# Performance work log

Hardware: AMD Instinct MI355X
Metric: run time of the kernel (lower is better)

## Reference

```python
import jax, jax.numpy as jnp
import numpy as np

B, S, D, H = 2, 2048, 1024, 16  # batch, seq_len, model dim, heads


def setup_inputs() -> dict:
    key = jax.random.key(0)
    ks = jax.random.split(key, 5)
    return {
        "x": jax.random.normal(ks[0], (B, S, D), jnp.float32),
        "idx": jax.random.randint(ks[1], (B,), 0, S),
        "weight": jnp.float32(0.5),
        "attn_forcing": 1,  # static python flag
        "w_qkv": jax.random.normal(ks[2], (D, 3 * D), jnp.float32) * 0.02,
        "b_qkv": jnp.zeros((3 * D,), jnp.float32),
        "w_proj": jax.random.normal(ks[3], (D, D), jnp.float32) * 0.02,
        "b_proj": jnp.zeros((D,), jnp.float32),
    }


def reference(x, idx, weight, attn_forcing, w_qkv, b_qkv, w_proj, b_proj):
    Bx, Sx, Dm = x.shape
    dh = Dm // H
    # qkv projection (Conv1D: x @ w + b)
    qkv = x @ w_qkv + b_qkv  # [B,S,3D]
    q, k, v = jnp.split(qkv, 3, axis=-1)
    q = q.reshape(Bx, Sx, H, dh).transpose(0, 2, 1, 3)  # [B,H,S,dh]
    k = k.reshape(Bx, Sx, H, dh).transpose(0, 2, 1, 3)
    v = v.reshape(Bx, Sx, H, dh).transpose(0, 2, 1, 3)
    alen = jnp.arange(Sx)
    mask = (alen[None, :] <= alen[:, None]).astype(x.dtype)  # [S,S] causal
    w = jnp.einsum('bhqd,bhkd->bhqk', q, k) / jnp.asarray(np.sqrt(dh), x.dtype)
    w = w * mask + jnp.asarray(-1e9, x.dtype) * (1 - mask)
    w = jax.nn.softmax(w, axis=-1)
    if attn_forcing:
        # post-softmax forcing reweight: positions >= idx scaled by weight, then renorm
        a = jnp.where(alen[None, :] >= idx[:, None], weight, jnp.asarray(1.0, x.dtype))  # [B,S]
        w = w * a[:, None, None, :]
        w = w / jnp.sum(w, axis=-1, keepdims=True)
    out = jnp.einsum('bhqk,bhkd->bhqd', w, v)  # [B,H,S,dh]
    out = out.transpose(0, 2, 1, 3).reshape(Bx, Sx, Dm)  # merge heads
    return out @ w_proj + b_proj
```

## Files before the change

kernel.cpp:

```cpp
#include <hip/hip_runtime.h>


typedef __attribute__((ext_vector_type(8))) short short8;
typedef __attribute__((ext_vector_type(4))) float f32x4;

#define MFMA_B16(a, b, c) __builtin_amdgcn_mfma_f32_16x16x32_bf16(a, b, c, 0, 0, 0)

static __device__ __forceinline__ unsigned short f2bf(float f) {
    union { float f; unsigned int u; } v;
    v.f = f;
    unsigned int r = (v.u + 0x7fffu + ((v.u >> 16) & 1u)) >> 16;
    return (unsigned short)r;
}

static __device__ __forceinline__ unsigned int pk_bf16(float a, float b) {
#if __has_builtin(__builtin_amdgcn_cvt_pk_bf16_f32)
    typedef __bf16 bf2 __attribute__((ext_vector_type(2)));
    union { bf2 v; unsigned int u; } c;
    c.v = __builtin_amdgcn_cvt_pk_bf16_f32(a, b);
    return c.u;
#else
    return (unsigned int)f2bf(a) | ((unsigned int)f2bf(b) << 16);
#endif
}

static __device__ __forceinline__ void gl_lds16(const void* g, void* l) {
    __builtin_amdgcn_global_load_lds(
        (const __attribute__((address_space(1))) unsigned int*)g,
        (__attribute__((address_space(3))) unsigned int*)l, 16, 0, 0);
}

__global__ __launch_bounds__(256) void convert_x_kernel(const float4* __restrict__ x,
                                                        ushort4* __restrict__ xb) {
    int i = blockIdx.x * 256 + threadIdx.x;
    float4 v = x[i];
    ushort4 o;
    o.x = f2bf(v.x); o.y = f2bf(v.y); o.z = f2bf(v.z); o.w = f2bf(v.w);
    xb[i] = o;
}

__global__ __launch_bounds__(256) void transpose_cvt_kernel(const float* __restrict__ in,
                                                            unsigned short* __restrict__ out,
                                                            int R, int C) {
    __shared__ float t[32][33];
    int c0 = blockIdx.x * 32, r0 = blockIdx.y * 32;
    int x = threadIdx.x, y = threadIdx.y;
    #pragma unroll
    for (int yy = y; yy < 32; yy += 8)
        t[yy][x] = in[(size_t)(r0 + yy) * C + (c0 + x)];
    __syncthreads();
    #pragma unroll
    for (int yy = y; yy < 32; yy += 8)
        out[(size_t)(c0 + yy) * R + (r0 + x)] = f2bf(t[x][yy]);
}

__global__ __launch_bounds__(256) void transpose_v_kernel(const unsigned short* __restrict__ v,
                                                          unsigned short* __restrict__ vT) {
    __shared__ unsigned short t[32][33];
    int d0 = blockIdx.x * 32, s0 = blockIdx.y * 32, bh = blockIdx.z;
    const unsigned short* vb = v + (size_t)bh * 2048 * 64;
    unsigned short* vTb = vT + (size_t)bh * 2048 * 64;
    int x = threadIdx.x, y = threadIdx.y;
    #pragma unroll
    for (int yy = y; yy < 32; yy += 8)
        t[yy][x] = vb[(s0 + yy) * 64 + d0 + x];
    __syncthreads();
    #pragma unroll
    for (int yy = y; yy < 32; yy += 8)
        vTb[(d0 + yy) * 2048 + s0 + x] = t[x][yy];
}

__global__ __launch_bounds__(256) void gemm_qkv_kernel(const unsigned short* __restrict__ A,
                                                       const unsigned short* __restrict__ Bt,
                                                       const float* __restrict__ bias,
                                                       unsigned short* __restrict__ q,
                                                       unsigned short* __restrict__ k,
                                                       unsigned short* __restrict__ v) {
    __shared__ unsigned short As[128 * 64];
    __shared__ unsigned short Bs[128 * 64];
    const int tid = threadIdx.x;
    const int lane = tid & 63, wave = tid >> 6;
    const int l15 = lane & 15, quad = lane >> 4;
    const int wm = wave >> 1, wn = wave & 1;
    const int row0 = blockIdx.y * 128, col0 = blockIdx.x * 128;
    const int K = 1024;

    int srow[4], scol[4], sdst[4];
    #pragma unroll
    for (int h = 0; h < 4; ++h) {
        int D = h * 256 + wave * 64 + lane;
        srow[h] = D >> 3;
        scol[h] = ((D & 7) ^ (srow[h] & 7)) * 8;
        sdst[h] = (h * 256 + wave * 64) * 8;
    }

    f32x4 acc[4][4] = {};

    for (int kt = 0; kt < K; kt += 64) {
        #pragma unroll
        for (int h = 0; h < 4; ++h) {
            gl_lds16(&A[(size_t)(row0 + srow[h]) * K + kt + scol[h]], &As[sdst[h]]);
            gl_lds16(&Bt[(size_t)(col0 + srow[h]) * K + kt + scol[h]], &Bs[sdst[h]]);
        }
        __syncthreads();
        #pragma unroll
        for (int kk = 0; kk < 2; ++kk) {
            short8 af[4], bf[4];
            #pragma unroll
            for (int i = 0; i < 4; ++i) {
                int r = wm * 64 + i * 16 + l15;
                af[i] = *(const short8*)&As[r * 64 + (((kk * 4 + quad) ^ (r & 7)) * 8)];
            }
            #pragma unroll
            for (int j = 0; j < 4; ++j) {
                int r = wn * 64 + j * 16 + l15;
                bf[j] = *(const short8*)&Bs[r * 64 + (((kk * 4 + quad) ^ (r & 7)) * 8)];
            }
            #pragma unroll
            for (int i = 0; i < 4; ++i)
                #pragma unroll
                for (int j = 0; j < 4; ++j)
                    acc[i][j] = MFMA_B16(af[i], bf[j], acc[i][j]);
        }
        __syncthreads();
    }

    #pragma unroll
    for (int i = 0; i < 4; ++i)
        #pragma unroll
        for (int j = 0; j < 4; ++j)
            #pragma unroll
            for (int r = 0; r < 4; ++r) {
                int row = row0 + wm * 64 + i * 16 + quad * 4 + r;
                int col = col0 + wn * 64 + j * 16 + l15;
                float val = acc[i][j][r] + bias[col];
                int which = col >> 10, rem = col & 1023;
                int hh = rem >> 6, d = rem & 63;
                int b = row >> 11, s = row & 2047;
                size_t o = ((size_t)((b * 16 + hh) * 2048 + s)) * 64 + d;
                if (which == 0) q[o] = f2bf(val * 0.125f);
                else if (which == 1) k[o] = f2bf(val);
                else v[o] = f2bf(val);
            }
}

__global__ __launch_bounds__(256) void gemm_proj_kernel(const unsigned short* __restrict__ A,
                                                        const unsigned short* __restrict__ Bt,
                                                        const float* __restrict__ bias,
                                                        float* __restrict__ out) {
    __shared__ unsigned short As[128 * 64];
    __shared__ unsigned short Bs[64 * 64];
    const int tid = threadIdx.x;
    const int lane = tid & 63, wave = tid >> 6;
    const int l15 = lane & 15, quad = lane >> 4;
    const int wm = wave >> 1, wn = wave & 1;
    const int row0 = blockIdx.y * 128, col0 = blockIdx.x * 64;
    const int K = 1024;

    int srow[4], scol[4], sdst[4];
    #pragma unroll
    for (int h = 0; h < 4; ++h) {
        int D = h * 256 + wave * 64 + lane;
        srow[h] = D >> 3;
        scol[h] = ((D & 7) ^ (srow[h] & 7)) * 8;
        sdst[h] = (h * 256 + wave * 64) * 8;
    }

    f32x4 acc[4][2] = {};

    for (int kt = 0; kt < K; kt += 64) {
        #pragma unroll
        for (int h = 0; h < 4; ++h)
            gl_lds16(&A[(size_t)(row0 + srow[h]) * K + kt + scol[h]], &As[sdst[h]]);
        #pragma unroll
        for (int h = 0; h < 2; ++h)
            gl_lds16(&Bt[(size_t)(col0 + srow[h]) * K + kt + scol[h]], &Bs[sdst[h]]);
        __syncthreads();
        #pragma unroll
        for (int kk = 0; kk < 2; ++kk) {
            short8 af[4], bf[2];
            #pragma unroll
            for (int i = 0; i < 4; ++i) {
                int r = wm * 64 + i * 16 + l15;
                af[i] = *(const short8*)&As[r * 64 + (((kk * 4 + quad) ^ (r & 7)) * 8)];
            }
            #pragma unroll
            for (int j = 0; j < 2; ++j) {
                int r = wn * 32 + j * 16 + l15;
                bf[j] = *(const short8*)&Bs[r * 64 + (((kk * 4 + quad) ^ (r & 7)) * 8)];
            }
            #pragma unroll
            for (int i = 0; i < 4; ++i)
                #pragma unroll
                for (int j = 0; j < 2; ++j)
                    acc[i][j] = MFMA_B16(af[i], bf[j], acc[i][j]);
        }
        __syncthreads();
    }

    #pragma unroll
    for (int i = 0; i < 4; ++i)
        #pragma unroll
        for (int j = 0; j < 2; ++j)
            #pragma unroll
            for (int r = 0; r < 4; ++r) {
                int row = row0 + wm * 64 + i * 16 + quad * 4 + r;
                int col = col0 + wn * 32 + j * 16 + l15;
                out[(size_t)row * 1024 + col] = acc[i][j][r] + bias[col];
            }
}

__global__ __launch_bounds__(256) void attn_kernel(const unsigned short* __restrict__ Q,
                                                   const unsigned short* __restrict__ Kg,
                                                   const unsigned short* __restrict__ Vt,
                                                   const int* __restrict__ idx,
                                                   const float* __restrict__ weight,
                                                   const int* __restrict__ forcing,
                                                   unsigned short* __restrict__ O) {
    __shared__ unsigned short Ks[2][4096];
    __shared__ unsigned short Vs[2][4096];
    __shared__ unsigned short Pw[4][1024];

    const int tid = threadIdx.x;
    const int lane = tid & 63, wave = tid >> 6;
    const int l15 = lane & 15, quad = lane >> 4;
    const int bid = blockIdx.x;
    const int u = bid >> 5, a = u & 7, qg = u >> 3;
    const int t = (qg == 0) ? (31 - a) : (qg == 1) ? (16 + a) : (qg == 2) ? (15 - a) : a;
    const int bh = bid & 31;
    const int b = bh >> 4, hh = bh & 15;
    const unsigned short* Qb = Q + (size_t)bh * 2048 * 64;
    const unsigned short* Kh = Kg + (size_t)bh * 2048 * 64;
    const unsigned short* Vh = Vt + (size_t)bh * 2048 * 64;

    const int idxb = idx[b];
    const float wgt = (forcing[0] != 0) ? weight[0] : 1.0f;

    const int L0 = wave * 128 + lane;
    const int rS = L0 >> 3;
    const int cS = (L0 & 7) ^ (rS & 7);
    const int ldsOffJ0 = (wave * 128) * 8;
    const int ldsOffJ1 = (wave * 128 + 64) * 8;

    const int q0 = t * 64 + wave * 16;
    const int qrow = q0 + l15;

    short8 aq0 = *(const short8*)&Qb[(q0 + l15) * 64 + quad * 8];
    short8 aq1 = *(const short8*)&Qb[(q0 + l15) * 64 + 32 + quad * 8];

    float m = -3.0e38f, l = 0.0f;
    f32x4 o[4] = {};

    const int nkb = t + 1;

    {
        const unsigned short* kg = Kh + (size_t)rS * 64 + cS * 8;
        const unsigned short* vg = Vh + (size_t)rS * 2048 + cS * 8;
        gl_lds16(kg,            &Ks[0][ldsOffJ0]);
        gl_lds16(kg + 8 * 64,   &Ks[0][ldsOffJ1]);
        gl_lds16(vg,            &Vs[0][ldsOffJ0]);
        gl_lds16(vg + 8 * 2048, &Vs[0][ldsOffJ1]);
    }
    __syncthreads();

    unsigned short* const pwb = &Pw[wave][0];
    const int pwr = l15 * 64;
    const int pa7 = l15 & 7;

    for (int kb = 0; kb < nkb; ++kb) {
        const int cur = kb & 1;
        const int kbase = kb * 64;
        if (kb + 1 < nkb) {
            const int nb = kbase + 64;
            const unsigned short* kg = Kh + (size_t)(nb + rS) * 64 + cS * 8;
            const unsigned short* vg = Vh + (size_t)rS * 2048 + nb + cS * 8;
            gl_lds16(kg,            &Ks[cur ^ 1][ldsOffJ0]);
            gl_lds16(kg + 8 * 64,   &Ks[cur ^ 1][ldsOffJ1]);
            gl_lds16(vg,            &Vs[cur ^ 1][ldsOffJ0]);
            gl_lds16(vg + 8 * 2048, &Vs[cur ^ 1][ldsOffJ1]);
        }

        f32x4 sT[4];
        #pragma unroll
        for (int kt = 0; kt < 4; ++kt) {
            const int row = kt * 16 + l15;
            short8 k0 = *(const short8*)&Ks[cur][row * 64 + ((quad ^ (row & 7)) * 8)];
            short8 k1 = *(const short8*)&Ks[cur][row * 64 + (((4 + quad) ^ (row & 7)) * 8)];
            f32x4 z = {};
            z = MFMA_B16(k0, aq0, z);
            z = MFMA_B16(k1, aq1, z);
            sT[kt] = z;
        }

        if (kb == t) {
            #pragma unroll
            for (int kt = 0; kt < 4; ++kt)
                #pragma unroll
                for (int r = 0; r < 4; ++r)
                    if (kbase + kt * 16 + quad * 4 + r > qrow) sT[kt][r] = -3.0e38f;
        }

        float mloc = fmaxf(fmaxf(fmaxf(sT[0][0], sT[0][1]), fmaxf(sT[0][2], sT[0][3])),
                           fmaxf(fmaxf(sT[1][0], sT[1][1]), fmaxf(sT[1][2], sT[1][3])));
        mloc = fmaxf(mloc, fmaxf(fmaxf(fmaxf(sT[2][0], sT[2][1]), fmaxf(sT[2][2], sT[2][3])),
                                 fmaxf(fmaxf(sT[3][0], sT[3][1]), fmaxf(sT[3][2], sT[3][3]))));
        mloc = fmaxf(mloc, __shfl_xor(mloc, 16));
        mloc = fmaxf(mloc, __shfl_xor(mloc, 32));
        const float mnew = fmaxf(m, mloc);
        const float alpha = __expf(m - mnew);
        m = mnew;

        #pragma unroll
        for (int kt = 0; kt < 4; ++kt)
            #pragma unroll
            for (int r = 0; r < 4; ++r)
                sT[kt][r] = __expf(sT[kt][r] - mnew);
        if (kbase >= idxb) {
            #pragma unroll
            for (int kt = 0; kt < 4; ++kt)
                #pragma unroll
                for (int r = 0; r < 4; ++r) sT[kt][r] *= wgt;
        } else if (kbase + 63 >= idxb) {
            #pragma unroll
            for (int kt = 0; kt < 4; ++kt)
                #pragma unroll
                for (int r = 0; r < 4; ++r)
                    if (kbase + kt * 16 + quad * 4 + r >= idxb) sT[kt][r] *= wgt;
        }

        float rs = ((sT[0][0] + sT[0][1]) + (sT[0][2] + sT[0][3])) +
                   ((sT[1][0] + sT[1][1]) + (sT[1][2] + sT[1][3])) +
                   ((sT[2][0] + sT[2][1]) + (sT[2][2] + sT[2][3])) +
                   ((sT[3][0] + sT[3][1]) + (sT[3][2] + sT[3][3]));
        rs += __shfl_xor(rs, 16);
        rs += __shfl_xor(rs, 32);
        l = l * alpha + rs;

        #pragma unroll
        for (int dt = 0; dt < 4; ++dt) {
            f32x4 tt = o[dt];
            #pragma unroll
            for (int r = 0; r < 4; ++r) tt[r] *= alpha;
            o[dt] = tt;
        }

        #pragma unroll
        for (int kt = 0; kt < 4; ++kt) {
            unsigned int* pw = (unsigned int*)&pwb[pwr +
                (((kt * 2 + (quad >> 1)) ^ pa7) * 8) + (quad & 1) * 4];
            pw[0] = pk_bf16(sT[kt][0], sT[kt][1]);
            pw[1] = pk_bf16(sT[kt][2], sT[kt][3]);
        }

        short8 bp0 = *(const short8*)&pwb[pwr + ((quad ^ pa7) * 8)];
        short8 bp1 = *(const short8*)&pwb[pwr + (((4 + quad) ^ pa7) * 8)];

        #pragma unroll
        for (int dt = 0; dt < 4; ++dt) {
            const int row = dt * 16 + l15;
            short8 vf0 = *(const short8*)&Vs[cur][row * 64 + ((quad ^ (row & 7)) * 8)];
            short8 vf1 = *(const short8*)&Vs[cur][row * 64 + (((4 + quad) ^ (row & 7)) * 8)];
            f32x4 oo = o[dt];
            oo = MFMA_B16(vf0, bp0, oo);
            oo = MFMA_B16(vf1, bp1, oo);
            o[dt] = oo;
        }

        __syncthreads();
    }

    const float inv = 1.0f / l;
    unsigned short* sc = &Ks[0][0] + wave * 1152;
    #pragma unroll
    for (int dt = 0; dt < 4; ++dt)
        #pragma unroll
        for (int r = 0; r < 4; ++r)
            sc[l15 * 72 + dt * 16 + quad * 4 + r] = f2bf(o[dt][r] * inv);
    const size_t rowoff = ((size_t)(b * 2048 + q0 + l15)) * 1024 + hh * 64;
    #pragma unroll
    for (int h = 0; h < 2; ++h) {
        short8 v8 = *(const short8*)&sc[l15 * 72 + quad * 16 + h * 8];
        *(short8*)&O[rowoff + quad * 16 + h * 8] = v8;
    }
}

extern "C" void kernel_launch(void* const* d_in, const int* in_sizes, int n_in,
                              void* d_out, int out_size, void* d_ws, size_t ws_size,
                              hipStream_t stream) {
    const float* x        = (const float*)d_in[0];
    const int*   idx      = (const int*)d_in[1];
    const float* weight   = (const float*)d_in[2];
    const int*   forcing  = (const int*)d_in[3];
    const float* w_qkv    = (const float*)d_in[4];
    const float* b_qkv    = (const float*)d_in[5];
    const float* w_proj   = (const float*)d_in[6];
    const float* b_proj   = (const float*)d_in[7];
    float* out = (float*)d_out;

    char* ws = (char*)d_ws;
    unsigned short* xb      = (unsigned short*)(ws);
    unsigned short* wqkvT   = (unsigned short*)(ws + 8388608);
    unsigned short* wprojT  = (unsigned short*)(ws + 14680064);
    unsigned short* qbuf    = (unsigned short*)(ws + 16777216);
    unsigned short* kbuf    = (unsigned short*)(ws + 25165824);
    unsigned short* vbuf    = (unsigned short*)(ws + 33554432);
    unsigned short* vTbuf   = (unsigned short*)(ws + 41943040);
    unsigned short* attn_out = xb;

    convert_x_kernel<<<4096, 256, 0, stream>>>((const float4*)x, (ushort4*)xb);
    transpose_cvt_kernel<<<dim3(96, 32), dim3(32, 8), 0, stream>>>(w_qkv, wqkvT, 1024, 3072);
    transpose_cvt_kernel<<<dim3(32, 32), dim3(32, 8), 0, stream>>>(w_proj, wprojT, 1024, 1024);
    gemm_qkv_kernel<<<dim3(24, 32), 256, 0, stream>>>(xb, wqkvT, b_qkv, qbuf, kbuf, vbuf);
    transpose_v_kernel<<<dim3(2, 64, 32), dim3(32, 8), 0, stream>>>(vbuf, vTbuf);
    attn_kernel<<<1024, 256, 0, stream>>>(qbuf, kbuf, vTbuf, idx, weight, forcing, attn_out);
    gemm_proj_kernel<<<dim3(16, 32), 256, 0, stream>>>(attn_out, wprojT, b_proj, out);
}
```

Measured before the change: 210.1 us.

## Fuse V transpose into QKV GEMM epilogue and drop online-softmax max tracking

```diff
diff --git a/kernel.cpp b/kernel.cpp
--- a/kernel.cpp
+++ b/kernel.cpp
@@ -5,6 +5,12 @@
 typedef __attribute__((ext_vector_type(4))) float f32x4;
 
 #define MFMA_B16(a, b, c) __builtin_amdgcn_mfma_f32_16x16x32_bf16(a, b, c, 0, 0, 0)
+
+#if __has_builtin(__builtin_amdgcn_exp2f)
+#define EXP2(x) __builtin_amdgcn_exp2f(x)
+#else
+#define EXP2(x) exp2f(x)
+#endif
 
 static __device__ __forceinline__ unsigned short f2bf(float f) {
     union { float f; unsigned int u; } v;
@@ -54,28 +60,12 @@
         out[(size_t)(c0 + yy) * R + (r0 + x)] = f2bf(t[x][yy]);
 }
 
-__global__ __launch_bounds__(256) void transpose_v_kernel(const unsigned short* __restrict__ v,
-                                                          unsigned short* __restrict__ vT) {
-    __shared__ unsigned short t[32][33];
-    int d0 = blockIdx.x * 32, s0 = blockIdx.y * 32, bh = blockIdx.z;
-    const unsigned short* vb = v + (size_t)bh * 2048 * 64;
-    unsigned short* vTb = vT + (size_t)bh * 2048 * 64;
-    int x = threadIdx.x, y = threadIdx.y;
-    #pragma unroll
-    for (int yy = y; yy < 32; yy += 8)
-        t[yy][x] = vb[(s0 + yy) * 64 + d0 + x];
-    __syncthreads();
-    #pragma unroll
-    for (int yy = y; yy < 32; yy += 8)
-        vTb[(d0 + yy) * 2048 + s0 + x] = t[x][yy];
-}
-
 __global__ __launch_bounds__(256) void gemm_qkv_kernel(const unsigned short* __restrict__ A,
                                                        const unsigned short* __restrict__ Bt,
                                                        const float* __restrict__ bias,
                                                        unsigned short* __restrict__ q,
                                                        unsigned short* __restrict__ k,
-                                                       unsigned short* __restrict__ v) {
+                                                       unsigned short* __restrict__ vT) {
     __shared__ unsigned short As[128 * 64];
     __shared__ unsigned short Bs[128 * 64];
     const int tid = threadIdx.x;
@@ -125,23 +115,54 @@
         __syncthreads();
     }
 
-    #pragma unroll
-    for (int i = 0; i < 4; ++i)
-        #pragma unroll
-        for (int j = 0; j < 4; ++j)
-            #pragma unroll
-            for (int r = 0; r < 4; ++r) {
-                int row = row0 + wm * 64 + i * 16 + quad * 4 + r;
-                int col = col0 + wn * 64 + j * 16 + l15;
-                float val = acc[i][j][r] + bias[col];
-                int which = col >> 10, rem = col & 1023;
-                int hh = rem >> 6, d = rem & 63;
-                int b = row >> 11, s = row & 2047;
-                size_t o = ((size_t)((b * 16 + hh) * 2048 + s)) * 64 + d;
-                if (which == 0) q[o] = f2bf(val * 0.125f);
-                else if (which == 1) k[o] = f2bf(val);
-                else v[o] = f2bf(val);
-            }
+    const int b = row0 >> 11;
+    const int srow0 = row0 & 2047;
+
+    if (blockIdx.x < 16) {
+        #pragma unroll
+        for (int i = 0; i < 4; ++i)
+            #pragma unroll
+            for (int j = 0; j < 4; ++j)
+                #pragma unroll
+                for (int r = 0; r < 4; ++r) {
+                    int row = row0 + wm * 64 + i * 16 + quad * 4 + r;
+                    int col = col0 + wn * 64 + j * 16 + l15;
+                    float val = acc[i][j][r] + bias[col];
+                    int which = col >> 10, rem = col & 1023;
+                    int hh = rem >> 6, d = rem & 63;
+                    int s = row & 2047;
+                    size_t o = ((size_t)((b * 16 + hh) * 2048 + s)) * 64 + d;
+                    if (which == 0) q[o] = f2bf(val * 0.1803368867f);
+                    else k[o] = f2bf(val);
+                }
+    } else {
+        unsigned short* tb = (wn == 0) ? As : Bs;
+        #pragma unroll
+        for (int i = 0; i < 4; ++i)
+            #pragma unroll
+            for (int j = 0; j < 4; ++j) {
+                const int col6 = j * 16 + l15;
+                const int gcol = col0 + wn * 64 + col6;
+                const float bb = bias[gcol];
+                const int chunk = wm * 8 + i * 2 + (quad >> 1);
+                unsigned int* pw = (unsigned int*)&tb[col6 * 128 +
+                    ((chunk ^ (col6 & 15)) * 8) + (quad & 1) * 4];
+                pw[0] = pk_bf16(acc[i][j][0] + bb, acc[i][j][1] + bb);
+                pw[1] = pk_bf16(acc[i][j][2] + bb, acc[i][j][3] + bb);
+            }
+        __syncthreads();
+        const int c = tid >> 1;
+        const int half = c >> 6, col6 = c & 63;
+        const int rhalf = (tid & 1) * 64;
+        const unsigned short* src = half ? Bs : As;
+        const int hh = (blockIdx.x - 16) * 2 + half;
+        unsigned short* dst = vT + ((size_t)((b * 16 + hh) * 64 + col6)) * 2048 + srow0 + rhalf;
+        #pragma unroll
+        for (int kk = 0; kk < 8; ++kk) {
+            const int chunk = ((rhalf >> 3) + kk) ^ (col6 & 15);
+            *(short8*)&dst[kk * 8] = *(const short8*)&src[col6 * 128 + chunk * 8];
+        }
+    }
 }
 
 __global__ __launch_bounds__(256) void gemm_proj_kernel(const unsigned short* __restrict__ A,
@@ -234,7 +255,7 @@
     const unsigned short* Vh = Vt + (size_t)bh * 2048 * 64;
 
     const int idxb = idx[b];
-    const float wgt = (forcing[0] != 0) ? weight[0] : 1.0f;
+    const float lw = (forcing[0] != 0) ? __log2f(weight[0]) : 0.0f;
 
     const int L0 = wave * 128 + lane;
     const int rS = L0 >> 3;
@@ -248,8 +269,10 @@
     short8 aq0 = *(const short8*)&Qb[(q0 + l15) * 64 + quad * 8];
     short8 aq1 = *(const short8*)&Qb[(q0 + l15) * 64 + 32 + quad * 8];
 
-    float m = -3.0e38f, l = 0.0f;
+    const short8 ones8 = {0x3F80, 0x3F80, 0x3F80, 0x3F80, 0x3F80, 0x3F80, 0x3F80, 0x3F80};
+
     f32x4 o[4] = {};
+    f32x4 lsum = {};
 
     const int nkb = t + 1;
 
@@ -280,13 +303,24 @@
             gl_lds16(vg + 8 * 2048, &Vs[cur ^ 1][ldsOffJ1]);
         }
 
+        const bool fullF = (kbase >= idxb);
+        const bool bndF = (!fullF) && (kbase + 63 >= idxb);
+        const float zu = fullF ? lw : 0.0f;
+
         f32x4 sT[4];
         #pragma unroll
         for (int kt = 0; kt < 4; ++kt) {
             const int row = kt * 16 + l15;
             short8 k0 = *(const short8*)&Ks[cur][row * 64 + ((quad ^ (row & 7)) * 8)];
             short8 k1 = *(const short8*)&Ks[cur][row * 64 + (((4 + quad) ^ (row & 7)) * 8)];
-            f32x4 z = {};
+            f32x4 z;
+            if (!bndF) {
+                z[0] = zu; z[1] = zu; z[2] = zu; z[3] = zu;
+            } else {
+                #pragma unroll
+                for (int r = 0; r < 4; ++r)
+                    z[r] = (kbase + kt * 16 + quad * 4 + r >= idxb) ? lw : 0.0f;
+            }
             z = MFMA_B16(k0, aq0, z);
             z = MFMA_B16(k1, aq1, z);
             sT[kt] = z;
@@ -300,49 +334,11 @@
                     if (kbase + kt * 16 + quad * 4 + r > qrow) sT[kt][r] = -3.0e38f;
         }
 
-        float mloc = fmaxf(fmaxf(fmaxf(sT[0][0], sT[0][1]), fmaxf(sT[0][2], sT[0][3])),
-                           fmaxf(fmaxf(sT[1][0], sT[1][1]), fmaxf(sT[1][2], sT[1][3])));
-        mloc = fmaxf(mloc, fmaxf(fmaxf(fmaxf(sT[2][0], sT[2][1]), fmaxf(sT[2][2], sT[2][3])),
-                                 fmaxf(fmaxf(sT[3][0], sT[3][1]), fmaxf(sT[3][2], sT[3][3]))));
-        mloc = fmaxf(mloc, __shfl_xor(mloc, 16));
-        mloc = fmaxf(mloc, __shfl_xor(mloc, 32));
-        const float mnew = fmaxf(m, mloc);
-        const float alpha = __expf(m - mnew);
-        m = mnew;
-
         #pragma unroll
         for (int kt = 0; kt < 4; ++kt)
             #pragma unroll
             for (int r = 0; r < 4; ++r)
-                sT[kt][r] = __expf(sT[kt][r] - mnew);
-        if (kbase >= idxb) {
-            #pragma unroll
-            for (int kt = 0; kt < 4; ++kt)
-                #pragma unroll
-                for (int r = 0; r < 4; ++r) sT[kt][r] *= wgt;
-        } else if (kbase + 63 >= idxb) {
-            #pragma unroll
-            for (int kt = 0; kt < 4; ++kt)
-                #pragma unroll
-                for (int r = 0; r < 4; ++r)
-                    if (kbase + kt * 16 + quad * 4 + r >= idxb) sT[kt][r] *= wgt;
-        }
-
-        float rs = ((sT[0][0] + sT[0][1]) + (sT[0][2] + sT[0][3])) +
-                   ((sT[1][0] + sT[1][1]) + (sT[1][2] + sT[1][3])) +
-                   ((sT[2][0] + sT[2][1]) + (sT[2][2] + sT[2][3])) +
-                   ((sT[3][0] + sT[3][1]) + (sT[3][2] + sT[3][3]));
-        rs += __shfl_xor(rs, 16);
-        rs += __shfl_xor(rs, 32);
-        l = l * alpha + rs;
-
-        #pragma unroll
-        for (int dt = 0; dt < 4; ++dt) {
-            f32x4 tt = o[dt];
-            #pragma unroll
-            for (int r = 0; r < 4; ++r) tt[r] *= alpha;
-            o[dt] = tt;
-        }
+                sT[kt][r] = EXP2(sT[kt][r]);
 
         #pragma unroll
         for (int kt = 0; kt < 4; ++kt) {
@@ -354,6 +350,9 @@
 
         short8 bp0 = *(const short8*)&pwb[pwr + ((quad ^ pa7) * 8)];
         short8 bp1 = *(const short8*)&pwb[pwr + (((4 + quad) ^ pa7) * 8)];
+
+        lsum = MFMA_B16(ones8, bp0, lsum);
+        lsum = MFMA_B16(ones8, bp1, lsum);
 
         #pragma unroll
         for (int dt = 0; dt < 4; ++dt) {
@@ -369,7 +368,7 @@
         __syncthreads();
     }
 
-    const float inv = 1.0f / l;
+    const float inv = 1.0f / lsum[0];
     unsigned short* sc = &Ks[0][0] + wave * 1152;
     #pragma unroll
     for (int dt = 0; dt < 4; ++dt)
@@ -403,15 +402,13 @@
     unsigned short* wprojT  = (unsigned short*)(ws + 14680064);
     unsigned short* qbuf    = (unsigned short*)(ws + 16777216);
     unsigned short* kbuf    = (unsigned short*)(ws + 25165824);
-    unsigned short* vbuf    = (unsigned short*)(ws + 33554432);
-    unsigned short* vTbuf   = (unsigned short*)(ws + 41943040);
+    unsigned short* vTbuf   = (unsigned short*)(ws + 33554432);
     unsigned short* attn_out = xb;
 
     convert_x_kernel<<<4096, 256, 0, stream>>>((const float4*)x, (ushort4*)xb);
     transpose_cvt_kernel<<<dim3(96, 32), dim3(32, 8), 0, stream>>>(w_qkv, wqkvT, 1024, 3072);
     transpose_cvt_kernel<<<dim3(32, 32), dim3(32, 8), 0, stream>>>(w_proj, wprojT, 1024, 1024);
-    gemm_qkv_kernel<<<dim3(24, 32), 256, 0, stream>>>(xb, wqkvT, b_qkv, qbuf, kbuf, vbuf);
-    transpose_v_kernel<<<dim3(2, 64, 32), dim3(32, 8), 0, stream>>>(vbuf, vTbuf);
+    gemm_qkv_kernel<<<dim3(24, 32), 256, 0, stream>>>(xb, wqkvT, b_qkv, qbuf, kbuf, vTbuf);
     attn_kernel<<<1024, 256, 0, stream>>>(qbuf, kbuf, vTbuf, idx, weight, forcing, attn_out);
     gemm_proj_kernel<<<dim3(16, 32), 256, 0, stream>>>(attn_out, wprojT, b_proj, out);
 }
```

After: 194.3 us. 7.5% less time.
